# Kernel optimization log

Measured on AMD Instinct MI355X. Metric: run time of the kernel, lower is better.

The kernel has to match this reference:

```python
import jax, jax.numpy as jnp
import numpy as np
from jax import lax

RATIO = 0.25
K = 16
EPS = 1e-5
B, N, CX, COUT, CAUX = 16, 4096, 64, 128, 32


def _fps(p, m):
    # Farthest point sampling on one cloud p:(N,3); deterministic start at index 0.
    mind = jnp.sum((p - p[0]) ** 2, axis=-1)  # (N,) min sq-dist to selected set
    def step(mind, _):
        nxt = jnp.argmax(mind)
        d = jnp.sum((p - p[nxt]) ** 2, axis=-1)
        return jnp.minimum(mind, d), nxt
    _, rest = lax.scan(step, mind, None, length=m - 1)
    return jnp.concatenate([jnp.zeros((1,), jnp.int32), rest.astype(jnp.int32)])


def setup_inputs() -> dict:
    key = jax.random.key(0)
    k1, k2, k3, k4, k5, k6 = jax.random.split(key, 6)
    P = B * N
    x = jax.random.normal(k1, (P, CX), jnp.float32)
    pos = jax.random.normal(k2, (P, 3), jnp.float32)
    batch = jnp.repeat(jnp.arange(B, dtype=jnp.int32), N)  # equal-size clouds
    aux = jax.random.normal(k3, (P, CAUX), jnp.float32)
    # MLP params: Linear(CX->COUT) + BatchNorm affine
    W = jax.random.normal(k4, (CX, COUT), jnp.float32) * (1.0 / np.sqrt(CX))
    b = jax.random.normal(k5, (COUT,), jnp.float32) * 0.02
    gamma = jnp.ones((COUT,), jnp.float32) + 0.1 * jax.random.normal(k6, (COUT,), jnp.float32)
    beta = jnp.zeros((COUT,), jnp.float32)
    return {"x": x, "pos": pos, "batch": batch, "aux": aux,
            "W": W, "b": b, "gamma": gamma, "beta": beta}


def reference(x, pos, batch, aux, W, b, gamma, beta):
    P = x.shape[0]
    nb = int(batch[-1]) + 1            # number of clouds (equal-size)
    n = P // nb
    m = int(n * RATIO)                 # clusters per cloud
    pos_b = pos.reshape(nb, n, 3)
    # --- FPS per cloud ---
    idx_local = jax.vmap(lambda p: _fps(p, m))(pos_b)                     # (B, M)
    id_clusters = (idx_local + jnp.arange(nb, dtype=jnp.int32)[:, None] * n).reshape(-1)
    centers = jnp.take_along_axis(pos_b, idx_local[..., None], axis=1)    # (B, M, 3)
    # --- kNN of all points to cluster centers, within each cloud ---
    d2 = jnp.sum((centers[:, :, None, :] - pos_b[:, None, :, :]) ** 2, axis=-1)  # (B, M, N)
    _, nb_local = lax.top_k(-d2, K)                                       # (B, M, K)
    nb_global = (nb_local + jnp.arange(nb, dtype=jnp.int32)[:, None, None] * n).reshape(-1)
    # --- MLP: Linear -> BatchNorm(batch stats, train mode) -> ReLU ---
    h = x @ W + b
    mu = jnp.mean(h, axis=0)
    var = jnp.var(h, axis=0)
    x_trans = jax.nn.relu(gamma * (h - mu) * lax.rsqrt(var + EPS) + beta)  # (P, Cout)
    # --- gather + per-cluster max / mean pooling (== scatter over knn edges) ---
    x_out = jnp.max(x_trans[nb_global].reshape(nb * m, K, -1), axis=1)     # (B*M, Cout)
    aux_out = jnp.mean(aux[nb_global].reshape(nb * m, K, -1), axis=1)      # (B*M, Caux)
    sub_pos = centers.reshape(-1, 3)
    sub_batch = batch[id_clusters]
    return x_out, sub_pos, sub_batch, aux_out, id_clusters
```

## Files before the change

### kernel.cpp

```cpp
#include <hip/hip_runtime.h>
#include <hip/hip_bf16.h>
#include <math.h>

#define NB    16
#define NPC   4096
#define MPC   1024
#define PTOT  65536
#define NCLU  16384
#define KNN_  16
#define CIN   64
#define COUT_ 128
#define CAUX_ 32

#define OFF_XOUT   0
#define OFF_SUBPOS (NCLU*COUT_)
#define OFF_SUBB   (OFF_SUBPOS + NCLU*3)
#define OFF_AUX    (OFF_SUBB + NCLU)
#define OFF_IDCL   (OFF_AUX + NCLU*CAUX_)

#define WS_H        0
#define WS_CENTERS  (PTOT*COUT_*4)
#define WS_STATS    (WS_CENTERS + NCLU*16)
#define WS_NEED     (WS_STATS + 256*4)

#define CAND_STRIDE 18
#define CAND_HALF   (16*CAND_STRIDE)
#define SM_LX    0
#define SM_LY    16384
#define SM_LZ    32768
#define SM_CAND  49152
#define SM_CST   53760
#define SM_XT    0
#define SM_WL    17408
#define SM_BS    50176
#define SM_BQ    50688
#define SM_SIZE  70144

__device__ __forceinline__ double dmax(double a, double b) { return __builtin_fmax(a, b); }
__device__ __forceinline__ double dmin(double a, double b) { return __builtin_fmin(a, b); }
__device__ __forceinline__ double pk(float d, int lo) {
  return __hiloint2double(__float_as_int(d), lo);
}
__device__ __forceinline__ int pk_lo(double k) {
  return (int)(unsigned)(__double_as_longlong(k) & 0xFFFFFFFFll);
}

template <int CTRL>
__device__ __forceinline__ double dpp64(double v) {
  long long u = __double_as_longlong(v);
  int lo = (int)(unsigned)(u & 0xFFFFFFFFll);
  int hi = (int)(unsigned)((unsigned long long)u >> 32);
  int rlo = __builtin_amdgcn_update_dpp(0, lo, CTRL, 0xf, 0xf, true);
  int rhi = __builtin_amdgcn_update_dpp(0, hi, CTRL, 0xf, 0xf, true);
  return __longlong_as_double(((long long)rhi << 32) | (long long)(unsigned)rlo);
}
#define ROR1 0x121
#define ROR2 0x122
#define ROR4 0x124
#define ROR8 0x128

__device__ __forceinline__ double tree16d(const double* p) {
  const double2* q = (const double2*)p;
  double2 q0 = q[0], q1 = q[1], q2 = q[2], q3 = q[3];
  double2 q4 = q[4], q5 = q[5], q6 = q[6], q7 = q[7];
  double a = dmax(dmax(dmax(q0.x, q0.y), dmax(q1.x, q1.y)),
                  dmax(dmax(q2.x, q2.y), dmax(q3.x, q3.y)));
  double b = dmax(dmax(dmax(q4.x, q4.y), dmax(q5.x, q5.y)),
                  dmax(dmax(q6.x, q6.y), dmax(q7.x, q7.y)));
  return dmax(a, b);
}

__device__ void fps_block(char* smem, const float* __restrict__ pos,
                          float4* __restrict__ centers, float* __restrict__ out)
{
  #pragma clang fp contract(off)
  float* lx = (float*)(smem + SM_LX);
  float* ly = (float*)(smem + SM_LY);
  float* lz = (float*)(smem + SM_LZ);
  double* cand = (double*)(smem + SM_CAND);
  float4* cst = (float4*)(smem + SM_CST);
  const int b = blockIdx.x;
  const int t = threadIdx.x;
  const float* pb = pos + (size_t)b * NPC * 3;
  const int myslot = (t >> 4) * CAND_STRIDE + (t & 15);
  const int rdbase = (t & 15) * CAND_STRIDE;

  float px[16], py[16], pz[16], mind[16];
  int lo16[16];
  {
    const float4* src = (const float4*)(pb + t * 48);
    float4 v[12];
    #pragma unroll
    for (int i = 0; i < 12; ++i) v[i] = src[i];
    const float* f = (const float*)v;
    #pragma unroll
    for (int j = 0; j < 16; ++j) {
      px[j] = f[3*j]; py[j] = f[3*j+1]; pz[j] = f[3*j+2];
      lx[t*16+j] = px[j]; ly[t*16+j] = py[j]; lz[t*16+j] = pz[j];
      lo16[j] = 4095 - (t*16 + j);
    }
  }
  __syncthreads();
  const float x0 = lx[0], y0 = ly[0], z0 = lz[0];
  if (t == 0) cst[0] = make_float4(x0, y0, z0, __int_as_float(0));

  double bk;
  {
    double k8[8];
    #pragma unroll
    for (int jp = 0; jp < 8; ++jp) {
      const int j0 = 2*jp, j1 = 2*jp + 1;
      float dx0 = px[j0]-x0, dy0 = py[j0]-y0, dz0 = pz[j0]-z0;
      float dx1 = px[j1]-x0, dy1 = py[j1]-y0, dz1 = pz[j1]-z0;
      float d0 = (dx0*dx0 + dy0*dy0) + dz0*dz0;
      float d1 = (dx1*dx1 + dy1*dy1) + dz1*dz1;
      mind[j0] = d0; mind[j1] = d1;
      k8[jp] = dmax(pk(d0, lo16[j0]), pk(d1, lo16[j1]));
    }
    double k40 = dmax(k8[0], k8[1]), k41 = dmax(k8[2], k8[3]);
    double k42 = dmax(k8[4], k8[5]), k43 = dmax(k8[6], k8[7]);
    bk = dmax(dmax(k40, k41), dmax(k42, k43));
  }

  for (int s = 1; s < MPC; ++s) {
    const int ph = (s & 1) * CAND_HALF;
    cand[ph + myslot] = bk;
    __syncthreads();
    double w = tree16d(cand + ph + rdbase);
    w = dmax(w, dpp64<ROR1>(w));
    w = dmax(w, dpp64<ROR2>(w));
    w = dmax(w, dpp64<ROR4>(w));
    w = dmax(w, dpp64<ROR8>(w));
    const int sel = 4095 - pk_lo(w);
    const float sx = lx[sel], sy = ly[sel], sz = lz[sel];
    if (t == 0) cst[s] = make_float4(sx, sy, sz, __int_as_float(sel));
    double k8[8];
    #pragma unroll
    for (int jp = 0; jp < 8; ++jp) {
      const int j0 = 2*jp, j1 = 2*jp + 1;
      float dx0 = px[j0]-sx, dy0 = py[j0]-sy, dz0 = pz[j0]-sz;
      float dx1 = px[j1]-sx, dy1 = py[j1]-sy, dz1 = pz[j1]-sz;
      float d0 = (dx0*dx0 + dy0*dy0) + dz0*dz0;
      float d1 = (dx1*dx1 + dy1*dy1) + dz1*dz1;
      float m0 = fminf(mind[j0], d0), m1 = fminf(mind[j1], d1);
      mind[j0] = m0; mind[j1] = m1;
      k8[jp] = dmax(pk(m0, lo16[j0]), pk(m1, lo16[j1]));
    }
    double k40 = dmax(k8[0], k8[1]), k41 = dmax(k8[2], k8[3]);
    double k42 = dmax(k8[4], k8[5]), k43 = dmax(k8[6], k8[7]);
    bk = dmax(dmax(k40, k41), dmax(k42, k43));
  }
  __syncthreads();
  for (int c = t; c < MPC; c += 256) {
    float4 q = cst[c];
    const int il = __float_as_int(q.w);
    const int cl = b*MPC + c;
    centers[cl] = make_float4(q.x, q.y, q.z, 0.0f);
    out[OFF_SUBPOS + cl*3 + 0] = q.x;
    out[OFF_SUBPOS + cl*3 + 1] = q.y;
    out[OFF_SUBPOS + cl*3 + 2] = q.z;
    out[OFF_SUBB + cl] = (float)b;
    out[OFF_IDCL + cl] = (float)(b*NPC + il);
  }
}

__device__ void gemm_block(char* smem, const float* __restrict__ x,
                           const float* __restrict__ W, const float* __restrict__ bias,
                           float* __restrict__ h, float* __restrict__ stats, int blk)
{
  float (*xT)[68]  = (float(*)[68])(smem + SM_XT);
  float (*Wl)[128] = (float(*)[128])(smem + SM_WL);
  float* bsum = (float*)(smem + SM_BS);
  float* bsq  = (float*)(smem + SM_BQ);
  const int t = threadIdx.x;
  const int row0 = blk * 64;
  if (t < 128) { bsum[t] = 0.0f; bsq[t] = 0.0f; }
  #pragma unroll
  for (int i = 0; i < 16; ++i) {
    const int idx = t + i*256;
    xT[idx & 63][idx >> 6] = x[(size_t)row0*64 + idx];
  }
  #pragma unroll
  for (int i = 0; i < 32; ++i) {
    const int idx = t + i*256;
    ((float*)Wl)[idx] = W[idx];
  }
  __syncthreads();
  const int tx = t & 15, ty = t >> 4;
  float acc[4][8] = {};
  #pragma unroll 8
  for (int k = 0; k < 64; ++k) {
    const float4 a  = *(const float4*)&xT[k][ty*4];
    const float4 b0 = *(const float4*)&Wl[k][tx*8];
    const float4 b1 = *(const float4*)&Wl[k][tx*8+4];
    const float av[4] = {a.x, a.y, a.z, a.w};
    const float bw[8] = {b0.x,b0.y,b0.z,b0.w,b1.x,b1.y,b1.z,b1.w};
    #pragma unroll
    for (int i2 = 0; i2 < 4; ++i2)
      #pragma unroll
      for (int e = 0; e < 8; ++e)
        acc[i2][e] += av[i2] * bw[e];
  }
  const int c0 = tx*8;
  float bb[8];
  #pragma unroll
  for (int e = 0; e < 8; ++e) bb[e] = bias[c0+e];
  float s8[8] = {}, q8[8] = {};
  #pragma unroll
  for (int i2 = 0; i2 < 4; ++i2) {
    float vv[8];
    #pragma unroll
    for (int e = 0; e < 8; ++e) {
      float v = acc[i2][e] + bb[e];
      vv[e] = v; s8[e] += v; q8[e] += v*v;
    }
    const int r = row0 + ty*4 + i2;
    float4* dst = (float4*)&h[(size_t)r*128 + c0];
    dst[0] = make_float4(vv[0], vv[1], vv[2], vv[3]);
    dst[1] = make_float4(vv[4], vv[5], vv[6], vv[7]);
  }
  #pragma unroll
  for (int e = 0; e < 8; ++e) {
    atomicAdd(&bsum[c0+e], s8[e]);
    atomicAdd(&bsq[c0+e],  q8[e]);
  }
  __syncthreads();
  if (t < 128) {
    atomicAdd(&stats[t],      bsum[t]);
    atomicAdd(&stats[128+t],  bsq[t]);
  }
}

__global__ __launch_bounds__(256) void fused_fps_gemm(const float* __restrict__ pos,
                                                      float4* __restrict__ centers,
                                                      float* __restrict__ out,
                                                      const float* __restrict__ x,
                                                      const float* __restrict__ W,
                                                      const float* __restrict__ bias,
                                                      float* __restrict__ h,
                                                      float* __restrict__ stats)
{
  __shared__ __align__(16) char smem[SM_SIZE];
  if (blockIdx.x < NB) fps_block(smem, pos, centers, out);
  else                 gemm_block(smem, x, W, bias, h, stats, blockIdx.x - NB);
}

#define KBIG __hiloint2double(0x7f7fffff, 0xffffffff)
#define CD_STRIDE 17

__global__ __launch_bounds__(256) void knn_pool(const float* __restrict__ pos,
                                                const float4* __restrict__ centers,
                                                const float* __restrict__ h,
                                                const float* __restrict__ aux,
                                                const float* __restrict__ stats,
                                                const float* __restrict__ gamma,
                                                const float* __restrict__ beta,
                                                float* __restrict__ out)
{
  #pragma clang fp contract(off)
  __shared__ float4 lp[NPC];
  __shared__ float  scl[128], ssh[128];
  __shared__ int    fid[32][16];
  const int blk = blockIdx.x;
  const int b   = blk >> 5;
  const int c0  = (blk & 31) * 32;
  const int t   = threadIdx.x;
  const int q   = t & 7;
  const int cc  = t >> 3;
  if (t < 128) {
    const float inv = 1.0f / 65536.0f;
    const float mu  = stats[t] * inv;
    const float var = stats[128+t] * inv - mu*mu;
    const float sc  = gamma[t] * rsqrtf(var + 1e-5f);
    scl[t] = sc;
    ssh[t] = beta[t] - mu*sc;
  }
  const float* pb = pos + (size_t)b * NPC * 3;
  for (int i = t; i < NPC; i += 256)
    lp[i] = make_float4(pb[3*i], pb[3*i+1], pb[3*i+2], 0.0f);
  __syncthreads();
  const int cg = b*MPC + c0 + cc;
  const float4 C = centers[cg];
  double L[16];
  #pragma unroll
  for (int k = 0; k < 16; ++k) L[k] = KBIG;
  for (int jj = 0; jj < NPC/8; ++jj) {
    const int j = jj*8 + q;
    const float4 p = lp[j];
    float dx = C.x - p.x, dy = C.y - p.y, dz = C.z - p.z;
    float d2 = (dx*dx + dy*dy) + dz*dz;
    double nk = pk(d2, j);
    if (nk < L[0]) {
      #pragma unroll
      for (int k = 0; k < 15; ++k) L[k] = dmin(L[k], dmax(L[k+1], nk));
      L[15] = dmin(L[15], nk);
    }
  }
  __syncthreads();
  double* cd = (double*)lp;
  #pragma unroll
  for (int k = 0; k < 16; ++k) cd[t*CD_STRIDE + k] = L[k];
  __syncthreads();
  if (q == 0) {
    double M[16];
    #pragma unroll
    for (int k = 0; k < 16; ++k) M[k] = KBIG;
    for (int ss = 0; ss < 8; ++ss) {
      const double* src = cd + (cc*8 + ss)*CD_STRIDE;
      #pragma unroll
      for (int k = 0; k < 16; ++k) {
        double nk = src[k];
        if (nk < M[0]) {
          #pragma unroll
          for (int m = 0; m < 15; ++m) M[m] = dmin(M[m], dmax(M[m+1], nk));
          M[15] = dmin(M[15], nk);
        }
      }
    }
    #pragma unroll
    for (int k = 0; k < 16; ++k) fid[cc][k] = b*NPC + pk_lo(M[k]);
  }
  __syncthreads();
  for (int g = 0; g < 16; ++g) {
    const int cc2 = g*2 + (t >> 7);
    const int col = t & 127;
    const int cl  = b*MPC + c0 + cc2;
    const float sc = scl[col], sh = ssh[col];
    float mv = 0.0f;
    #pragma unroll
    for (int k = 0; k < 16; ++k) {
      const float hv = h[(size_t)fid[cc2][k]*128 + col];
      mv = fmaxf(mv, fmaxf(sc*hv + sh, 0.0f));
    }
    out[OFF_XOUT + (size_t)cl*128 + col] = mv;
    if (col < 32) {
      float s = 0.0f;
      #pragma unroll
      for (int k = 0; k < 16; ++k) s += aux[(size_t)fid[cc2][k]*32 + col];
      out[OFF_AUX + (size_t)cl*32 + col] = s * (1.0f/16.0f);
    }
  }
}

extern "C" void kernel_launch(void* const* d_in, const int* in_sizes, int n_in,
                              void* d_out, int out_size, void* d_ws, size_t ws_size,
                              hipStream_t stream)
{
  const float* x     = (const float*)d_in[0];
  const float* pos   = (const float*)d_in[1];
  const float* aux   = (const float*)d_in[3];
  const float* W     = (const float*)d_in[4];
  const float* bias  = (const float*)d_in[5];
  const float* gamma = (const float*)d_in[6];
  const float* beta  = (const float*)d_in[7];
  float* out = (float*)d_out;
  char*  ws  = (char*)d_ws;
  if (ws_size < (size_t)WS_NEED) return;

  float*  h       = (float*)(ws + WS_H);
  float4* centers = (float4*)(ws + WS_CENTERS);
  float*  stats   = (float*)(ws + WS_STATS);

  hipMemsetAsync(stats, 0, 256*4, stream);
  hipLaunchKernelGGL(fused_fps_gemm, dim3(NB + PTOT/64), dim3(256), 0, stream,
                     pos, centers, out, x, W, bias, h, stats);
  hipLaunchKernelGGL(knn_pool, dim3(512), dim3(256), 0, stream,
                     pos, centers, h, aux, stats, gamma, beta, out);
}
```

Baseline: 828.8 us.

## Double FPS block to 512 threads with two-level wave-row argmax reduction

```diff
diff --git a/kernel.cpp b/kernel.cpp
--- a/kernel.cpp
+++ b/kernel.cpp
@@ -23,18 +23,16 @@
 #define WS_STATS    (WS_CENTERS + NCLU*16)
 #define WS_NEED     (WS_STATS + 256*4)
 
-#define CAND_STRIDE 18
-#define CAND_HALF   (16*CAND_STRIDE)
 #define SM_LX    0
 #define SM_LY    16384
 #define SM_LZ    32768
 #define SM_CAND  49152
-#define SM_CST   53760
+#define SM_CSEL  49664
 #define SM_XT    0
 #define SM_WL    17408
 #define SM_BS    50176
 #define SM_BQ    50688
-#define SM_SIZE  70144
+#define SM_SIZE  53760
 
 __device__ __forceinline__ double dmax(double a, double b) { return __builtin_fmax(a, b); }
 __device__ __forceinline__ double dmin(double a, double b) { return __builtin_fmin(a, b); }
@@ -59,15 +57,12 @@
 #define ROR4 0x124
 #define ROR8 0x128
 
-__device__ __forceinline__ double tree16d(const double* p) {
-  const double2* q = (const double2*)p;
-  double2 q0 = q[0], q1 = q[1], q2 = q[2], q3 = q[3];
-  double2 q4 = q[4], q5 = q[5], q6 = q[6], q7 = q[7];
-  double a = dmax(dmax(dmax(q0.x, q0.y), dmax(q1.x, q1.y)),
-                  dmax(dmax(q2.x, q2.y), dmax(q3.x, q3.y)));
-  double b = dmax(dmax(dmax(q4.x, q4.y), dmax(q5.x, q5.y)),
-                  dmax(dmax(q6.x, q6.y), dmax(q7.x, q7.y)));
-  return dmax(a, b);
+__device__ __forceinline__ double rowmax16(double w) {
+  w = dmax(w, dpp64<ROR1>(w));
+  w = dmax(w, dpp64<ROR2>(w));
+  w = dmax(w, dpp64<ROR4>(w));
+  w = dmax(w, dpp64<ROR8>(w));
+  return w;
 }
 
 __device__ void fps_block(char* smem, const float* __restrict__ pos,
@@ -78,65 +73,61 @@
   float* ly = (float*)(smem + SM_LY);
   float* lz = (float*)(smem + SM_LZ);
   double* cand = (double*)(smem + SM_CAND);
-  float4* cst = (float4*)(smem + SM_CST);
+  int*   csel = (int*)(smem + SM_CSEL);
   const int b = blockIdx.x;
   const int t = threadIdx.x;
   const float* pb = pos + (size_t)b * NPC * 3;
-  const int myslot = (t >> 4) * CAND_STRIDE + (t & 15);
-  const int rdbase = (t & 15) * CAND_STRIDE;
-
-  float px[16], py[16], pz[16], mind[16];
-  int lo16[16];
+  const int entry  = (t >> 6) * 4 + ((t >> 4) & 3);
+  const bool writer = ((t & 15) == 0);
+
+  float px[8], py[8], pz[8], mind[8];
+  int lo8[8];
   {
-    const float4* src = (const float4*)(pb + t * 48);
-    float4 v[12];
-    #pragma unroll
-    for (int i = 0; i < 12; ++i) v[i] = src[i];
+    const float4* src = (const float4*)(pb + t * 24);
+    float4 v[6];
+    #pragma unroll
+    for (int i = 0; i < 6; ++i) v[i] = src[i];
     const float* f = (const float*)v;
     #pragma unroll
-    for (int j = 0; j < 16; ++j) {
+    for (int j = 0; j < 8; ++j) {
       px[j] = f[3*j]; py[j] = f[3*j+1]; pz[j] = f[3*j+2];
-      lx[t*16+j] = px[j]; ly[t*16+j] = py[j]; lz[t*16+j] = pz[j];
-      lo16[j] = 4095 - (t*16 + j);
+      lx[t*8+j] = px[j]; ly[t*8+j] = py[j]; lz[t*8+j] = pz[j];
+      lo8[j] = 4095 - (t*8 + j);
     }
   }
   __syncthreads();
   const float x0 = lx[0], y0 = ly[0], z0 = lz[0];
-  if (t == 0) cst[0] = make_float4(x0, y0, z0, __int_as_float(0));
+  if (t == 0) csel[0] = 0;
 
   double bk;
   {
-    double k8[8];
-    #pragma unroll
-    for (int jp = 0; jp < 8; ++jp) {
+    double k4[4];
+    #pragma unroll
+    for (int jp = 0; jp < 4; ++jp) {
       const int j0 = 2*jp, j1 = 2*jp + 1;
       float dx0 = px[j0]-x0, dy0 = py[j0]-y0, dz0 = pz[j0]-z0;
       float dx1 = px[j1]-x0, dy1 = py[j1]-y0, dz1 = pz[j1]-z0;
       float d0 = (dx0*dx0 + dy0*dy0) + dz0*dz0;
       float d1 = (dx1*dx1 + dy1*dy1) + dz1*dz1;
       mind[j0] = d0; mind[j1] = d1;
-      k8[jp] = dmax(pk(d0, lo16[j0]), pk(d1, lo16[j1]));
-    }
-    double k40 = dmax(k8[0], k8[1]), k41 = dmax(k8[2], k8[3]);
-    double k42 = dmax(k8[4], k8[5]), k43 = dmax(k8[6], k8[7]);
-    bk = dmax(dmax(k40, k41), dmax(k42, k43));
+      k4[jp] = dmax(pk(d0, lo8[j0]), pk(d1, lo8[j1]));
+    }
+    bk = dmax(dmax(k4[0], k4[1]), dmax(k4[2], k4[3]));
   }
 
   for (int s = 1; s < MPC; ++s) {
-    const int ph = (s & 1) * CAND_HALF;
-    cand[ph + myslot] = bk;
+    double w = rowmax16(bk);
+    const int ph = (s & 1) * 32;
+    if (writer) cand[ph + entry] = w;
     __syncthreads();
-    double w = tree16d(cand + ph + rdbase);
-    w = dmax(w, dpp64<ROR1>(w));
-    w = dmax(w, dpp64<ROR2>(w));
-    w = dmax(w, dpp64<ROR4>(w));
-    w = dmax(w, dpp64<ROR8>(w));
-    const int sel = 4095 - pk_lo(w);
+    double2 pr = ((const double2*)(cand + ph))[t & 15];
+    double w2 = rowmax16(dmax(pr.x, pr.y));
+    const int sel = 4095 - pk_lo(w2);
     const float sx = lx[sel], sy = ly[sel], sz = lz[sel];
-    if (t == 0) cst[s] = make_float4(sx, sy, sz, __int_as_float(sel));
-    double k8[8];
-    #pragma unroll
-    for (int jp = 0; jp < 8; ++jp) {
+    if (t == 0) csel[s] = sel;
+    double k4[4];
+    #pragma unroll
+    for (int jp = 0; jp < 4; ++jp) {
       const int j0 = 2*jp, j1 = 2*jp + 1;
       float dx0 = px[j0]-sx, dy0 = py[j0]-sy, dz0 = pz[j0]-sz;
       float dx1 = px[j1]-sx, dy1 = py[j1]-sy, dz1 = pz[j1]-sz;
@@ -144,21 +135,19 @@
       float d1 = (dx1*dx1 + dy1*dy1) + dz1*dz1;
       float m0 = fminf(mind[j0], d0), m1 = fminf(mind[j1], d1);
       mind[j0] = m0; mind[j1] = m1;
-      k8[jp] = dmax(pk(m0, lo16[j0]), pk(m1, lo16[j1]));
-    }
-    double k40 = dmax(k8[0], k8[1]), k41 = dmax(k8[2], k8[3]);
-    double k42 = dmax(k8[4], k8[5]), k43 = dmax(k8[6], k8[7]);
-    bk = dmax(dmax(k40, k41), dmax(k42, k43));
-  }
-  __syncthreads();
-  for (int c = t; c < MPC; c += 256) {
-    float4 q = cst[c];
-    const int il = __float_as_int(q.w);
+      k4[jp] = dmax(pk(m0, lo8[j0]), pk(m1, lo8[j1]));
+    }
+    bk = dmax(dmax(k4[0], k4[1]), dmax(k4[2], k4[3]));
+  }
+  __syncthreads();
+  for (int c = t; c < MPC; c += 512) {
+    const int il = csel[c];
     const int cl = b*MPC + c;
-    centers[cl] = make_float4(q.x, q.y, q.z, 0.0f);
-    out[OFF_SUBPOS + cl*3 + 0] = q.x;
-    out[OFF_SUBPOS + cl*3 + 1] = q.y;
-    out[OFF_SUBPOS + cl*3 + 2] = q.z;
+    const float X = lx[il], Y = ly[il], Z = lz[il];
+    centers[cl] = make_float4(X, Y, Z, 0.0f);
+    out[OFF_SUBPOS + cl*3 + 0] = X;
+    out[OFF_SUBPOS + cl*3 + 1] = Y;
+    out[OFF_SUBPOS + cl*3 + 2] = Z;
     out[OFF_SUBB + cl] = (float)b;
     out[OFF_IDCL + cl] = (float)(b*NPC + il);
   }
@@ -176,53 +165,50 @@
   const int row0 = blk * 64;
   if (t < 128) { bsum[t] = 0.0f; bsq[t] = 0.0f; }
   #pragma unroll
+  for (int i = 0; i < 8; ++i) {
+    const int idx = t + i*512;
+    xT[idx & 63][idx >> 6] = x[(size_t)row0*64 + idx];
+  }
+  #pragma unroll
   for (int i = 0; i < 16; ++i) {
-    const int idx = t + i*256;
-    xT[idx & 63][idx >> 6] = x[(size_t)row0*64 + idx];
-  }
-  #pragma unroll
-  for (int i = 0; i < 32; ++i) {
-    const int idx = t + i*256;
+    const int idx = t + i*512;
     ((float*)Wl)[idx] = W[idx];
   }
   __syncthreads();
-  const int tx = t & 15, ty = t >> 4;
-  float acc[4][8] = {};
+  const int tx = t & 31, ty = t >> 5;
+  float acc[4][4] = {};
   #pragma unroll 8
   for (int k = 0; k < 64; ++k) {
     const float4 a  = *(const float4*)&xT[k][ty*4];
-    const float4 b0 = *(const float4*)&Wl[k][tx*8];
-    const float4 b1 = *(const float4*)&Wl[k][tx*8+4];
+    const float4 b0 = *(const float4*)&Wl[k][tx*4];
     const float av[4] = {a.x, a.y, a.z, a.w};
-    const float bw[8] = {b0.x,b0.y,b0.z,b0.w,b1.x,b1.y,b1.z,b1.w};
+    const float bw[4] = {b0.x, b0.y, b0.z, b0.w};
     #pragma unroll
     for (int i2 = 0; i2 < 4; ++i2)
       #pragma unroll
-      for (int e = 0; e < 8; ++e)
+      for (int e = 0; e < 4; ++e)
         acc[i2][e] += av[i2] * bw[e];
   }
-  const int c0 = tx*8;
-  float bb[8];
-  #pragma unroll
-  for (int e = 0; e < 8; ++e) bb[e] = bias[c0+e];
-  float s8[8] = {}, q8[8] = {};
+  const int c0 = tx*4;
+  float bb[4];
+  #pragma unroll
+  for (int e = 0; e < 4; ++e) bb[e] = bias[c0+e];
+  float s4[4] = {}, q4[4] = {};
   #pragma unroll
   for (int i2 = 0; i2 < 4; ++i2) {
-    float vv[8];
-    #pragma unroll
-    for (int e = 0; e < 8; ++e) {
+    float vv[4];
+    #pragma unroll
+    for (int e = 0; e < 4; ++e) {
       float v = acc[i2][e] + bb[e];
-      vv[e] = v; s8[e] += v; q8[e] += v*v;
+      vv[e] = v; s4[e] += v; q4[e] += v*v;
     }
     const int r = row0 + ty*4 + i2;
-    float4* dst = (float4*)&h[(size_t)r*128 + c0];
-    dst[0] = make_float4(vv[0], vv[1], vv[2], vv[3]);
-    dst[1] = make_float4(vv[4], vv[5], vv[6], vv[7]);
-  }
-  #pragma unroll
-  for (int e = 0; e < 8; ++e) {
-    atomicAdd(&bsum[c0+e], s8[e]);
-    atomicAdd(&bsq[c0+e],  q8[e]);
+    *(float4*)&h[(size_t)r*128 + c0] = make_float4(vv[0], vv[1], vv[2], vv[3]);
+  }
+  #pragma unroll
+  for (int e = 0; e < 4; ++e) {
+    atomicAdd(&bsum[c0+e], s4[e]);
+    atomicAdd(&bsq[c0+e],  q4[e]);
   }
   __syncthreads();
   if (t < 128) {
@@ -231,7 +217,7 @@
   }
 }
 
-__global__ __launch_bounds__(256) void fused_fps_gemm(const float* __restrict__ pos,
+__global__ __launch_bounds__(512) void fused_fps_gemm(const float* __restrict__ pos,
                                                       float4* __restrict__ centers,
                                                       float* __restrict__ out,
                                                       const float* __restrict__ x,
@@ -362,7 +348,7 @@
   float*  stats   = (float*)(ws + WS_STATS);
 
   hipMemsetAsync(stats, 0, 256*4, stream);
-  hipLaunchKernelGGL(fused_fps_gemm, dim3(NB + PTOT/64), dim3(256), 0, stream,
+  hipLaunchKernelGGL(fused_fps_gemm, dim3(NB + PTOT/64), dim3(512), 0, stream,
                      pos, centers, out, x, W, bias, h, stats);
   hipLaunchKernelGGL(knn_pool, dim3(512), dim3(256), 0, stream,
                      pos, centers, h, aux, stats, gamma, beta, out);
```

Result: faster. 762.2 us (-8.0%).
